# Kernel optimization log

Hardware: AMD Instinct MI355X
Metric: run time of the kernel (lower is better)

Reference implementation:

```python
import jax, jax.numpy as jnp
import numpy as np

D_MODEL = 2048
H = 16
D_K = D_MODEL // H


def setup_inputs() -> dict:
    key = jax.random.key(0)
    ks = jax.random.split(key, 9)
    b, n, d = 2, 2048, D_MODEL
    s = 1.0 / np.sqrt(d)
    return {
        "x": jax.random.normal(ks[0], (b, n, d), jnp.float32),
        "Wq": jax.random.normal(ks[1], (d, d), jnp.float32) * s,
        "bq": jax.random.normal(ks[2], (d,), jnp.float32) * 0.01,
        "Wk": jax.random.normal(ks[3], (d, d), jnp.float32) * s,
        "bk": jax.random.normal(ks[4], (d,), jnp.float32) * 0.01,
        "Wv": jax.random.normal(ks[5], (d, d), jnp.float32) * s,
        "bv": jax.random.normal(ks[6], (d,), jnp.float32) * 0.01,
        "Wo": jax.random.normal(ks[7], (d, d), jnp.float32) * s,
        "bo": jax.random.normal(ks[8], (d,), jnp.float32) * 0.01,
    }


def reference(x, Wq, bq, Wk, bk, Wv, bv, Wo, bo):
    b, n, d = x.shape
    h, dk = H, D_K

    def split_heads(t):
        return t.reshape(b, n, h, dk).transpose(0, 2, 1, 3)  # (b,h,n,dk)

    q = split_heads(x @ Wq + bq)
    k = split_heads(x @ Wk + bk)
    v = split_heads(x @ Wv + bv)

    scores = jnp.einsum("bhqd,bhkd->bhqk", q, k) / jnp.sqrt(jnp.float32(dk))
    causal = jnp.tril(jnp.ones((n, n), dtype=bool))  # (n,n)
    scores = jnp.where(causal[None, None], scores, -jnp.inf)
    attn = jax.nn.softmax(scores, axis=-1)  # dropout = identity (eval)

    out = jnp.einsum("bhqk,bhkd->bhqd", attn, v)
    out = out.transpose(0, 2, 1, 3).reshape(b, n, d)
    return out @ Wo + bo
```

## Files before the change

kernel.cpp:

```cpp
#include <hip/hip_runtime.h>

typedef unsigned short u16;
typedef unsigned int u32;
typedef __attribute__((ext_vector_type(8))) short short8;
typedef __attribute__((ext_vector_type(4))) float f32x4;
typedef __attribute__((ext_vector_type(16))) float f32x16;
typedef __attribute__((ext_vector_type(4))) u16 u16x4;
typedef __attribute__((ext_vector_type(4))) u32 u32x4;

#define QK_SCALE 0.12751736915185197f

__device__ __forceinline__ u16 f2bf(float f) {
  u32 u = __builtin_bit_cast(u32, f);
  u = u + 0x7FFFu + ((u >> 16) & 1u);
  return (u16)(u >> 16);
}

__device__ __forceinline__ void async_copy16(const void* g, void* l) {
  __builtin_amdgcn_global_load_lds(
      (const __attribute__((address_space(1))) u32*)g,
      (__attribute__((address_space(3))) u32*)l, 16, 0, 0);
}

#define VMCNT(n) asm volatile("s_waitcnt vmcnt(" #n ")" ::: "memory")

__global__ __launch_bounds__(256) void cast_x_kernel(const float* __restrict__ x,
                                                     u16* __restrict__ xb, int n) {
  int i = (blockIdx.x * 256 + threadIdx.x) * 8;
  if (i >= n) return;
  float4 a = *(const float4*)(x + i);
  float4 b = *(const float4*)(x + i + 4);
  short8 o;
  o[0] = (short)f2bf(a.x); o[1] = (short)f2bf(a.y);
  o[2] = (short)f2bf(a.z); o[3] = (short)f2bf(a.w);
  o[4] = (short)f2bf(b.x); o[5] = (short)f2bf(b.y);
  o[6] = (short)f2bf(b.z); o[7] = (short)f2bf(b.w);
  *(short8*)(xb + i) = o;
}

__global__ __launch_bounds__(256) void transW_kernel(
    const float* __restrict__ W0, const float* __restrict__ W1,
    const float* __restrict__ W2, const float* __restrict__ W3,
    u16* __restrict__ O0, u16* __restrict__ O1, u16* __restrict__ O2, u16* __restrict__ O3) {
  const float* Ws[4] = {W0, W1, W2, W3};
  u16* Os[4] = {O0, O1, O2, O3};
  const float* W = Ws[blockIdx.z];
  u16* O = Os[blockIdx.z];

  __shared__ float T[64][65];
  int t = threadIdx.x;
  int k0 = blockIdx.y * 64, n0 = blockIdx.x * 64;
  int r = t >> 4, c = (t & 15) * 4;
#pragma unroll
  for (int i = 0; i < 4; ++i) {
    float4 v = *(const float4*)&W[(size_t)(k0 + r + i * 16) * 2048 + n0 + c];
    T[r + i * 16][c + 0] = v.x; T[r + i * 16][c + 1] = v.y;
    T[r + i * 16][c + 2] = v.z; T[r + i * 16][c + 3] = v.w;
  }
  __syncthreads();
#pragma unroll
  for (int i = 0; i < 4; ++i) {
    int nn = r + i * 16;
    u16x4 o;
    o[0] = f2bf(T[c + 0][nn]); o[1] = f2bf(T[c + 1][nn]);
    o[2] = f2bf(T[c + 2][nn]); o[3] = f2bf(T[c + 3][nn]);
    *(u16x4*)&O[(size_t)(n0 + nn) * 2048 + k0 + c] = o;
  }
}

__global__ __launch_bounds__(512, 2) void gemm192_kernel(
    const u16* __restrict__ A, const u16* __restrict__ W,
    const float* __restrict__ b0, const float* __restrict__ b1, const float* __restrict__ b2,
    u16* __restrict__ oq, u16* __restrict__ ok, u16* __restrict__ ovt) {
  __shared__ __align__(16) u16 SM[57344];

  int t = threadIdx.x;
  int lane = t & 63, w = t >> 6;
  int wm = w >> 2, wn = w & 3;
  int g = lane >> 4, lr = lane & 15;
  int m0 = blockIdx.y * 256, n0 = blockIdx.x * 192;

  const u16* AsrcB = A + (size_t)(m0 + (t >> 3)) * 2048 + ((t & 7) ^ ((t >> 3) & 7)) * 8;
  const u16* BsrcB = W + (size_t)(n0 + (t >> 3)) * 2048 + ((t & 7) ^ ((t >> 3) & 7)) * 8;
  int t8 = t * 8;

  int ko0 = (g ^ (lr & 7)) * 8;
  int ko1 = ((4 + g) ^ (lr & 7)) * 8;
  int aoff[8], boff[3];
#pragma unroll
  for (int mf = 0; mf < 8; ++mf) aoff[mf] = (wm * 128 + mf * 16 + lr) * 64;
#pragma unroll
  for (int nf = 0; nf < 3; ++nf) boff[nf] = 16384 + (wn * 48 + nf * 16 + lr) * 64;

  f32x4 acc[8][3] = {};
  short8 af[2][2], bfr[3][2];

#define SA(bb, j, tl) \
  async_copy16(AsrcB + (size_t)(j) * 131072 + (tl) * 64, (void*)(SM + (bb) * 28672 + (j) * 4096 + t8))
#define SB(bb, j, tl) \
  async_copy16(BsrcB + (size_t)(j) * 131072 + (tl) * 64, \
               (void*)(SM + (bb) * 28672 + 16384 + (j) * 4096 + t8))

#define PHASE(hbuf, q, STAGE_OPS, VM_OP)                                        \
  {                                                                             \
    const u16* Ab = SM + (hbuf) * 28672;                                        \
    af[0][0] = *(const short8*)&Ab[aoff[2 * (q)] + ko0];                        \
    af[0][1] = *(const short8*)&Ab[aoff[2 * (q)] + ko1];                        \
    af[1][0] = *(const short8*)&Ab[aoff[2 * (q) + 1] + ko0];                    \
    af[1][1] = *(const short8*)&Ab[aoff[2 * (q) + 1] + ko1];                    \
    if ((q) == 0) {                                                             \
      _Pragma("unroll") for (int nf = 0; nf < 3; ++nf) {                        \
        bfr[nf][0] = *(const short8*)&Ab[boff[nf] + ko0];                       \
        bfr[nf][1] = *(const short8*)&Ab[boff[nf] + ko1];                       \
      }                                                                         \
    }                                                                           \
    STAGE_OPS;                                                                  \
    __builtin_amdgcn_s_barrier();                                               \
    asm volatile("s_waitcnt lgkmcnt(0)" ::: "memory");                          \
    __builtin_amdgcn_sched_barrier(0);                                          \
    __builtin_amdgcn_s_setprio(1);                                              \
    _Pragma("unroll") for (int kk = 0; kk < 2; ++kk)                            \
        _Pragma("unroll") for (int m2 = 0; m2 < 2; ++m2)                        \
            _Pragma("unroll") for (int nf = 0; nf < 3; ++nf)                    \
                acc[2 * (q) + m2][nf] = __builtin_amdgcn_mfma_f32_16x16x32_bf16(\
                    af[m2][kk], bfr[nf][kk], acc[2 * (q) + m2][nf], 0, 0, 0);   \
    __builtin_amdgcn_s_setprio(0);                                              \
    VM_OP;                                                                      \
    __builtin_amdgcn_s_barrier();                                               \
  }

  SB(0, 0, 0); SB(0, 1, 0); SB(0, 2, 0);
  SA(0, 0, 0); SA(0, 1, 0); SA(0, 2, 0); SA(0, 3, 0);
  SB(1, 0, 1); SB(1, 1, 1); SB(1, 2, 1);
  SA(1, 0, 1); SA(1, 2, 1);
  VMCNT(5);
  __builtin_amdgcn_s_barrier();

  for (int i = 0; i < 16; ++i) {
    bool more = i < 15;
    int t1 = 2 * i + 1, t2 = 2 * i + 2, t3 = 2 * i + 3;
    PHASE(0, 0, { SA(1, 1, t1); SA(1, 3, t1); }, {});
    PHASE(0, 1, { if (more) { SB(0, 0, t2); SB(0, 1, t2); } }, {});
    PHASE(0, 2, { if (more) { SB(0, 2, t2); SA(0, 0, t2); } }, {});
    PHASE(0, 3, { if (more) { SA(0, 2, t2); } },
          { if (more) { VMCNT(5); } else { VMCNT(0); } });
    PHASE(1, 0, { if (more) { SA(0, 1, t2); SA(0, 3, t2); } }, {});
    PHASE(1, 1, { if (more) { SB(1, 0, t3); SB(1, 1, t3); } }, {});
    PHASE(1, 2, { if (more) { SB(1, 2, t3); SA(1, 0, t3); } }, {});
    PHASE(1, 3, { if (more) { SA(1, 2, t3); } },
          { if (more) { VMCNT(5); } else { VMCNT(0); } });
  }
#undef PHASE
#undef SA
#undef SB

  bool hasV = (n0 + 191) >= 4096;
#pragma unroll
  for (int mf = 0; mf < 8; ++mf) {
#pragma unroll
    for (int nf = 0; nf < 3; ++nf) {
      int colc = wn * 48 + nf * 16 + lr;
      int col = n0 + colc;
      int z = col >> 11;
      int cc = col & 2047;
      if (z < 2) {
        float bv = (z == 0 ? b0 : b1)[cc];
        u16* outb = (z == 0) ? oq : ok;
#pragma unroll
        for (int i = 0; i < 4; ++i) {
          int rr = m0 + wm * 128 + mf * 16 + 4 * g + i;
          int b = rr >> 11, np = rr & 2047, h = cc >> 7, dk = cc & 127;
          outb[((size_t)(b * 16 + h) * 2048 + np) * 128 + dk] = f2bf(acc[mf][nf][i] + bv);
        }
      } else {
        float bv = b2[cc];
#pragma unroll
        for (int i = 0; i < 4; ++i) {
          int token = wm * 128 + mf * 16 + 4 * g + i;
          SM[colc * 264 + token] = f2bf(acc[mf][nf][i] + bv);
        }
      }
    }
  }
  if (hasV) {
    __syncthreads();
    int b = m0 >> 11;
    int npb = m0 & 2047;
#pragma unroll
    for (int it = 0; it < 12; ++it) {
      int id = t + 512 * it;
      int colc = id >> 5;
      int c8 = (id & 31) * 8;
      int col = n0 + colc;
      if (col >= 4096) {
        short8 v = *(const short8*)&SM[colc * 264 + c8];
        int vcol = col - 4096;
        int h = vcol >> 7, dk = vcol & 127;
        *(short8*)&ovt[(((size_t)(b * 16 + h) * 128 + dk) * 2048) + npb + c8] = v;
      }
    }
  }
}

__global__ __launch_bounds__(512, 2) void gemmO_kernel(
    const u16* __restrict__ A, const u16* __restrict__ W,
    const float* __restrict__ bias, float* __restrict__ of) {
  __shared__ __align__(16) u16 SM[73728];

  int t = threadIdx.x;
  int lane = t & 63, w = t >> 6;
  int wm = w >> 2, wn = w & 3;
  int g = lane >> 4, lr = lane & 15;
  int m0 = blockIdx.y * 128, n0 = blockIdx.x * 256;

  int sArow = ((t >> 8) << 6) + ((t >> 3) & 31);
  int c8A = (t & 7) ^ ((t >> 3) & 7);
  const u16* Asrc = A + (size_t)(m0 + sArow) * 2048 + c8A * 8;
  int rB = t >> 3;
  int c8B = (t & 7) ^ (rB & 7);
  const u16* Bsrc = W + (size_t)(n0 + rB) * 2048 + c8B * 8;

  int ko0 = (g ^ (lr & 7)) * 8;
  int ko1 = ((4 + g) ^ (lr & 7)) * 8;
  int offA[4], offB[4];
#pragma unroll
  for (int mf = 0; mf < 4; ++mf)
    offA[mf] = (mf >> 1) * 4096 + wm * 2048 + ((mf & 1) * 16 + lr) * 64;
#pragma unroll
  for (int nf = 0; nf < 4; ++nf)
    offB[nf] = 8192 + (wn >> 1) * 8192 + ((wn & 1) * 64 + nf * 16 + lr) * 64;

  f32x4 acc[4][4] = {};

#define STG_A(sbuf, mh, kt) \
  async_copy16(Asrc + (mh) * 65536 + (kt), (void*)(SM + (sbuf) + (mh) * 4096 + t * 8))
#define STG_B(sbuf, half, kt)                                                 \
  do {                                                                        \
    async_copy16(Bsrc + (half) * 262144 + (kt),                               \
                 (void*)(SM + (sbuf) + 8192 + (half) * 8192 + t * 8));        \
    async_copy16(Bsrc + (half) * 262144 + 131072 + (kt),                      \
                 (void*)(SM + (sbuf) + 8192 + (half) * 8192 + 4096 + t * 8)); \
  } while (0)

  STG_A(0, 0, 0); STG_B(0, 0, 0);
  STG_A(0, 1, 0); STG_B(0, 1, 0);
  STG_A(24576, 0, 64); STG_B(24576, 0, 64);
  STG_A(24576, 1, 64); STG_B(24576, 1, 64);
  VMCNT(6);
  __builtin_amdgcn_s_barrier();

  u32 cb = 0, sb = 49152;
  for (int tt = 0; tt < 32; ++tt) {
    int kt2 = (tt + 2) << 6;
    bool stg = tt < 30;
    const u16* Bu = SM + cb;

    short8 af[2][2], bfr[4][2];
#pragma unroll
    for (int m2 = 0; m2 < 2; ++m2) {
      af[m2][0] = *(const short8*)&Bu[offA[m2] + ko0];
      af[m2][1] = *(const short8*)&Bu[offA[m2] + ko1];
    }
#pragma unroll
    for (int nf = 0; nf < 4; ++nf) {
      bfr[nf][0] = *(const short8*)&Bu[offB[nf] + ko0];
      bfr[nf][1] = *(const short8*)&Bu[offB[nf] + ko1];
    }
    if (stg) { STG_A(sb, 0, kt2); STG_B(sb, 0, kt2); }
    __builtin_amdgcn_s_barrier();
    asm volatile("s_waitcnt lgkmcnt(0)" ::: "memory");
    __builtin_amdgcn_sched_barrier(0);
    __builtin_amdgcn_s_setprio(1);
#pragma unroll
    for (int kk = 0; kk < 2; ++kk)
#pragma unroll
      for (int m2 = 0; m2 < 2; ++m2)
#pragma unroll
        for (int nf = 0; nf < 4; ++nf)
          acc[m2][nf] =
              __builtin_amdgcn_mfma_f32_16x16x32_bf16(af[m2][kk], bfr[nf][kk], acc[m2][nf], 0, 0, 0);
    __builtin_amdgcn_s_setprio(0);
    __builtin_amdgcn_s_barrier();

#pragma unroll
    for (int m2 = 0; m2 < 2; ++m2) {
      af[m2][0] = *(const short8*)&Bu[offA[2 + m2] + ko0];
      af[m2][1] = *(const short8*)&Bu[offA[2 + m2] + ko1];
    }
    if (stg) { STG_A(sb, 1, kt2); STG_B(sb, 1, kt2); }
    __builtin_amdgcn_s_barrier();
    asm volatile("s_waitcnt lgkmcnt(0)" ::: "memory");
    __builtin_amdgcn_sched_barrier(0);
    __builtin_amdgcn_s_setprio(1);
#pragma unroll
    for (int kk = 0; kk < 2; ++kk)
#pragma unroll
      for (int m2 = 0; m2 < 2; ++m2)
#pragma unroll
        for (int nf = 0; nf < 4; ++nf)
          acc[2 + m2][nf] = __builtin_amdgcn_mfma_f32_16x16x32_bf16(af[m2][kk], bfr[nf][kk],
                                                                    acc[2 + m2][nf], 0, 0, 0);
    __builtin_amdgcn_s_setprio(0);
    if (tt < 30) { VMCNT(6); } else { VMCNT(0); }
    __builtin_amdgcn_s_barrier();

    cb += 24576; if (cb == 73728) cb = 0;
    sb += 24576; if (sb == 73728) sb = 0;
  }
#undef STG_A
#undef STG_B

#pragma unroll
  for (int mf = 0; mf < 4; ++mf) {
#pragma unroll
    for (int nf = 0; nf < 4; ++nf) {
      int col = n0 + wn * 64 + nf * 16 + lr;
      float bv = bias[col];
#pragma unroll
      for (int i = 0; i < 4; ++i) {
        int rr = m0 + wm * 64 + mf * 16 + 4 * g + i;
        of[(size_t)rr * 2048 + col] = acc[mf][nf][i] + bv;
      }
    }
  }
}

__global__ __launch_bounds__(256, 2) void attn_kernel(
    const u16* __restrict__ Q, const u16* __restrict__ K, const u16* __restrict__ Vt,
    u16* __restrict__ ctx) {
  int bh = blockIdx.y;
  int q0 = (int)(gridDim.x - 1 - blockIdx.x) * 128;
  int t = threadIdx.x, lane = t & 63, w = t >> 6;
  int h = lane >> 5;
  int ql = lane & 31;
  int q0w = q0 + w * 32;
  int qg = q0w + ql;

  const u16* Qb = Q + (size_t)bh * 262144;
  const u16* Kb = K + (size_t)bh * 262144;
  const u16* Vb = Vt + (size_t)bh * 262144;

  __shared__ __align__(16) u16 SM[32768];

  short8 qf[8];
  {
    const u16* qrow = Qb + (size_t)qg * 128 + 8 * h;
#pragma unroll
    for (int kk = 0; kk < 8; ++kk) qf[kk] = *(const short8*)(qrow + 16 * kk);
  }

  f32x16 acc[4] = {};
  float m = -1e30f, lsum = 0.f;

  int nt = (q0 + 128) >> 6;
  int wave_max = q0w + 31;

  auto STAGE = [&](int buf, int kv0) {
    u16* Ksb = SM + buf * 16384;
    u16* Vsb = Ksb + 8192;
#pragma unroll
    for (int it = 0; it < 4; ++it) {
      int p = t + 256 * it;
      int row = p >> 4;
      int c = (p & 15) ^ (row & 15);
      async_copy16(Kb + (size_t)(kv0 + row) * 128 + c * 8, (void*)(Ksb + p * 8));
      async_copy16(Vb + (size_t)(2 * row + (c >> 3)) * 2048 + kv0 + (c & 7) * 8,
                   (void*)(Vsb + p * 8));
    }
  };

  STAGE(0, 0);
  __syncthreads();

  for (int step = 0; step < nt; ++step) {
    int kv0 = step << 6;
    int cur = step & 1;
    if (step + 1 < nt) STAGE(cur ^ 1, (step + 1) << 6);

    if (kv0 <= wave_max) {
      const u16* Ksb = SM + cur * 16384;
      const u16* Vsb = Ksb + 8192;

      f32x16 s0 = {}, s1 = {};
      __builtin_amdgcn_s_setprio(1);
#pragma unroll
      for (int kk = 0; kk < 8; ++kk) {
        int c = (2 * kk + h) ^ (ql & 15);
        short8 kf0 = *(const short8*)&Ksb[ql * 128 + c * 8];
        s0 = __builtin_amdgcn_mfma_f32_32x32x16_bf16(kf0, qf[kk], s0, 0, 0, 0);
        short8 kf1 = *(const short8*)&Ksb[(32 + ql) * 128 + c * 8];
        s1 = __builtin_amdgcn_mfma_f32_32x32x16_bf16(kf1, qf[kk], s1, 0, 0, 0);
      }
      __builtin_amdgcn_s_setprio(0);

      if (kv0 + 63 > q0w) {
#pragma unroll
        for (int r = 0; r < 16; ++r) {
          int slot = (r & 3) + 8 * (r >> 2) + 4 * h;
          if (kv0 + slot > qg) s0[r] = -1e30f;
          if (kv0 + 32 + slot > qg) s1[r] = -1e30f;
        }
      }

      float tm = fmaxf(s0[0], s1[0]);
#pragma unroll
      for (int r = 1; r < 16; ++r) tm = fmaxf(tm, fmaxf(s0[r], s1[r]));
      tm = fmaxf(tm, __shfl_xor(tm, 32));
      tm *= QK_SCALE;

      if (__any(tm > m + 8.0f)) {
        float mn = fmaxf(m, tm);
        float rr = exp2f(m - mn);
        m = mn;
        lsum *= rr;
#pragma unroll
        for (int d = 0; d < 4; ++d)
#pragma unroll
          for (int i = 0; i < 16; ++i) acc[d][i] *= rr;
      }

      float rs = 0.f;
#pragma unroll
      for (int r = 0; r < 16; ++r) {
        s0[r] = exp2f(fmaf(s0[r], QK_SCALE, -m));
        s1[r] = exp2f(fmaf(s1[r], QK_SCALE, -m));
        rs += s0[r] + s1[r];
      }
      rs += __shfl_xor(rs, 32);
      lsum += rs;

      u32 up0[8], up1[8];
#pragma unroll
      for (int mi = 0; mi < 8; ++mi) {
        asm("v_cvt_pk_bf16_f32 %0, %1, %2" : "=v"(up0[mi]) : "v"(s0[2 * mi]), "v"(s0[2 * mi + 1]));
        asm("v_cvt_pk_bf16_f32 %0, %1, %2" : "=v"(up1[mi]) : "v"(s1[2 * mi]), "v"(s1[2 * mi + 1]));
      }

#pragma unroll
      for (int g16 = 0; g16 < 4; ++g16) {
        int Qd = g16 & 1;
        u32 c0 = (g16 < 2) ? up0[4 * Qd + 0] : up1[4 * Qd + 0];
        u32 c1 = (g16 < 2) ? up0[4 * Qd + 1] : up1[4 * Qd + 1];
        u32 c2 = (g16 < 2) ? up0[4 * Qd + 2] : up1[4 * Qd + 2];
        u32 c3 = (g16 < 2) ? up0[4 * Qd + 3] : up1[4 * Qd + 3];
        u32 d0 = __shfl_xor(c0, 32), d1 = __shfl_xor(c1, 32);
        u32 d2 = __shfl_xor(c2, 32), d3 = __shfl_xor(c3, 32);
        u32x4 paw;
        paw[0] = h ? d2 : c0;
        paw[1] = h ? d3 : c1;
        paw[2] = h ? c2 : d0;
        paw[3] = h ? c3 : d1;
        short8 pa = __builtin_bit_cast(short8, paw);
        __builtin_amdgcn_s_setprio(1);
#pragma unroll
        for (int d = 0; d < 4; ++d) {
          int dk = 32 * d + ql;
          int prow = dk >> 1;
          int lch = (dk & 1) * 8 + 2 * g16 + h;
          int slot = lch ^ (prow & 15);
          short8 vf = *(const short8*)&Vsb[prow * 128 + slot * 8];
          acc[d] = __builtin_amdgcn_mfma_f32_32x32x16_bf16(vf, pa, acc[d], 0, 0, 0);
        }
        __builtin_amdgcn_s_setprio(0);
      }
    }
    __syncthreads();
  }

  u16* Ot = SM + w * 4352;
  float inv = 1.f / lsum;
#pragma unroll
  for (int d = 0; d < 4; ++d)
#pragma unroll
    for (int r = 0; r < 16; ++r) {
      int dk = 32 * d + (r & 3) + 8 * (r >> 2) + 4 * h;
      Ot[ql * 136 + dk] = f2bf(acc[d][r] * inv);
    }
  __syncthreads();
  int b = bh >> 4, hh = bh & 15;
#pragma unroll
  for (int it = 0; it < 8; ++it) {
    int p = lane + 64 * it;
    int row = p >> 4, ch = p & 15;
    short8 v = *(const short8*)&Ot[row * 136 + ch * 8];
    *(short8*)(ctx + ((size_t)(b * 2048 + q0 + w * 32 + row)) * 2048 + hh * 128 + ch * 8) = v;
  }
}

extern "C" void kernel_launch(void* const* d_in, const int* in_sizes, int n_in,
                              void* d_out, int out_size, void* d_ws, size_t ws_size,
                              hipStream_t stream) {
  const float* x = (const float*)d_in[0];
  const float* Wq = (const float*)d_in[1];
  const float* bq = (const float*)d_in[2];
  const float* Wk = (const float*)d_in[3];
  const float* bk = (const float*)d_in[4];
  const float* Wv = (const float*)d_in[5];
  const float* bv = (const float*)d_in[6];
  const float* Wo = (const float*)d_in[7];
  const float* bo = (const float*)d_in[8];
  float* out = (float*)d_out;

  u16* xb = (u16*)d_ws;
  u16* WTq = xb + 8388608;
  u16* WTk = WTq + 4194304;
  u16* WTv = WTk + 4194304;
  u16* WTo = WTv + 4194304;
  u16* Qs = WTo + 4194304;
  u16* Ks = Qs + 8388608;
  u16* Vt = Ks + 8388608;
  u16* ctx = Vt + 8388608;

  cast_x_kernel<<<4096, 256, 0, stream>>>(x, xb, 8388608);
  transW_kernel<<<dim3(32, 32, 4), 256, 0, stream>>>(Wq, Wk, Wv, Wo, WTq, WTk, WTv, WTo);
  gemm192_kernel<<<dim3(32, 16), 512, 0, stream>>>(xb, WTq, bq, bk, bv, Qs, Ks, Vt);
  attn_kernel<<<dim3(16, 32), 256, 0, stream>>>(Qs, Ks, Vt, ctx);
  gemmO_kernel<<<dim3(8, 32), 512, 0, stream>>>(ctx, WTo, bo, out);
}
```

Measured before the change: 250.5 us.

## Merge QKV GEMM K-loop phases into two halves with fewer barriers

Restructures the pipelined bf16 GEMM main loop from four phases per K-tile (two M-fragments each) into two phases covering four M-fragments each. It drops the mid-phase barrier and regroups the async global-to-LDS stage issues, adjusting the vmcnt waits to match. This is meant to cut barrier and synchronization overhead and give larger MFMA bursts per phase. In exchange it raises register pressure for the A fragments and changes the hazard ordering between LDS writes and reads, which could break correctness if the waits are wrong.

```diff
diff --git a/kernel.cpp b/kernel.cpp
--- a/kernel.cpp
+++ b/kernel.cpp
@@ -93,7 +93,7 @@
   for (int nf = 0; nf < 3; ++nf) boff[nf] = 16384 + (wn * 48 + nf * 16 + lr) * 64;
 
   f32x4 acc[8][3] = {};
-  short8 af[2][2], bfr[3][2];
+  short8 bfr[3][2];
 
 #define SA(bb, j, tl) \
   async_copy16(AsrcB + (size_t)(j) * 131072 + (tl) * 64, (void*)(SM + (bb) * 28672 + (j) * 4096 + t8))
@@ -101,29 +101,29 @@
   async_copy16(BsrcB + (size_t)(j) * 131072 + (tl) * 64, \
                (void*)(SM + (bb) * 28672 + 16384 + (j) * 4096 + t8))
 
-#define PHASE(hbuf, q, STAGE_OPS, VM_OP)                                        \
+#define PH(bufofs, half, STAGE_OPS, VM_OP)                                      \
   {                                                                             \
-    const u16* Ab = SM + (hbuf) * 28672;                                        \
-    af[0][0] = *(const short8*)&Ab[aoff[2 * (q)] + ko0];                        \
-    af[0][1] = *(const short8*)&Ab[aoff[2 * (q)] + ko1];                        \
-    af[1][0] = *(const short8*)&Ab[aoff[2 * (q) + 1] + ko0];                    \
-    af[1][1] = *(const short8*)&Ab[aoff[2 * (q) + 1] + ko1];                    \
-    if ((q) == 0) {                                                             \
+    const u16* Ab = SM + (bufofs);                                              \
+    short8 af[4][2];                                                            \
+    _Pragma("unroll") for (int mf = 0; mf < 4; ++mf) {                          \
+      af[mf][0] = *(const short8*)&Ab[aoff[4 * (half) + mf] + ko0];             \
+      af[mf][1] = *(const short8*)&Ab[aoff[4 * (half) + mf] + ko1];             \
+    }                                                                           \
+    if ((half) == 0) {                                                          \
       _Pragma("unroll") for (int nf = 0; nf < 3; ++nf) {                        \
         bfr[nf][0] = *(const short8*)&Ab[boff[nf] + ko0];                       \
         bfr[nf][1] = *(const short8*)&Ab[boff[nf] + ko1];                       \
       }                                                                         \
     }                                                                           \
     STAGE_OPS;                                                                  \
-    __builtin_amdgcn_s_barrier();                                               \
     asm volatile("s_waitcnt lgkmcnt(0)" ::: "memory");                          \
     __builtin_amdgcn_sched_barrier(0);                                          \
     __builtin_amdgcn_s_setprio(1);                                              \
     _Pragma("unroll") for (int kk = 0; kk < 2; ++kk)                            \
-        _Pragma("unroll") for (int m2 = 0; m2 < 2; ++m2)                        \
+        _Pragma("unroll") for (int mf = 0; mf < 4; ++mf)                        \
             _Pragma("unroll") for (int nf = 0; nf < 3; ++nf)                    \
-                acc[2 * (q) + m2][nf] = __builtin_amdgcn_mfma_f32_16x16x32_bf16(\
-                    af[m2][kk], bfr[nf][kk], acc[2 * (q) + m2][nf], 0, 0, 0);   \
+                acc[4 * (half) + mf][nf] = __builtin_amdgcn_mfma_f32_16x16x32_bf16(\
+                    af[mf][kk], bfr[nf][kk], acc[4 * (half) + mf][nf], 0, 0, 0);\
     __builtin_amdgcn_s_setprio(0);                                              \
     VM_OP;                                                                      \
     __builtin_amdgcn_s_barrier();                                               \
@@ -139,18 +139,17 @@
   for (int i = 0; i < 16; ++i) {
     bool more = i < 15;
     int t1 = 2 * i + 1, t2 = 2 * i + 2, t3 = 2 * i + 3;
-    PHASE(0, 0, { SA(1, 1, t1); SA(1, 3, t1); }, {});
-    PHASE(0, 1, { if (more) { SB(0, 0, t2); SB(0, 1, t2); } }, {});
-    PHASE(0, 2, { if (more) { SB(0, 2, t2); SA(0, 0, t2); } }, {});
-    PHASE(0, 3, { if (more) { SA(0, 2, t2); } },
-          { if (more) { VMCNT(5); } else { VMCNT(0); } });
-    PHASE(1, 0, { if (more) { SA(0, 1, t2); SA(0, 3, t2); } }, {});
-    PHASE(1, 1, { if (more) { SB(1, 0, t3); SB(1, 1, t3); } }, {});
-    PHASE(1, 2, { if (more) { SB(1, 2, t3); SA(1, 0, t3); } }, {});
-    PHASE(1, 3, { if (more) { SA(1, 2, t3); } },
-          { if (more) { VMCNT(5); } else { VMCNT(0); } });
-  }
-#undef PHASE
+    PH(0, 0, { SA(1, 1, t1); SA(1, 3, t1); }, { VMCNT(7); });
+    PH(0, 1,
+       { if (more) { SB(0, 0, t2); SB(0, 1, t2); SB(0, 2, t2); SA(0, 0, t2); SA(0, 2, t2); } },
+       { if (more) { VMCNT(7); } else { VMCNT(2); } });
+    PH(28672, 0, { if (more) { SA(0, 1, t2); SA(0, 3, t2); } },
+       { if (more) { VMCNT(7); } else { VMCNT(0); } });
+    PH(28672, 1,
+       { if (more) { SB(1, 0, t3); SB(1, 1, t3); SB(1, 2, t3); SA(1, 0, t3); SA(1, 2, t3); } },
+       { if (more) { VMCNT(7); } });
+  }
+#undef PH
 #undef SA
 #undef SB
 
```

Measured after the change: 248.1 us. About the same (-1.0%).
